# Performance work log

Hardware: AMD Instinct MI355X
Metric: run time of the kernel (lower is better)

## Reference

```python
import jax, jax.numpy as jnp
import numpy as np

HEADS = 16
EPS = 1e-5  # nn.LayerNorm default


def setup_inputs() -> dict:
    key = jax.random.key(0)
    ks = jax.random.split(key, 3)
    b, n, dim = 4, 1024, 1024
    x = jax.random.normal(ks[0], (b, n, dim), jnp.float32)
    ln_gamma = jnp.ones((dim,), jnp.float32)
    ln_beta = jnp.zeros((dim,), jnp.float32)
    # torch.nn.Linear stores weight as [out_features, in_features]
    w_qkv = jax.random.normal(ks[1], (3 * dim, dim), jnp.float32) * (dim ** -0.5)
    w_out = jax.random.normal(ks[2], (dim, dim), jnp.float32) * (dim ** -0.5)
    b_out = jnp.zeros((dim,), jnp.float32)
    return {"x": x, "ln_gamma": ln_gamma, "ln_beta": ln_beta,
            "w_qkv": w_qkv, "w_out": w_out, "b_out": b_out, "topk": 32}


def reference(x, ln_gamma, ln_beta, w_qkv, w_out, b_out, topk):
    b, n, dim = x.shape
    h = HEADS
    d = dim // h
    scale = d ** -0.5  # (inner_dim/heads)^-0.5 with inner_dim=dim

    # LayerNorm (biased variance, matching torch)
    mu = x.mean(-1, keepdims=True)
    var = x.var(-1, keepdims=True)
    xn = (x - mu) * jax.lax.rsqrt(var + EPS) * ln_gamma + ln_beta

    # qkv projection (no bias): y = x @ W^T
    qkv = jnp.einsum('bnd,ed->bne', xn, w_qkv)  # [b, n, 3*dim]
    q, k, v = jnp.split(qkv, 3, axis=-1)
    split_heads = lambda t: t.reshape(b, n, h, d).transpose(0, 2, 1, 3)  # [b,h,n,d]
    q = split_heads(q) * scale
    k = split_heads(k)
    v = split_heads(v)

    sim = jnp.einsum('bhid,bhjd->bhij', q, k)          # [b,h,n,n]
    attn = jax.nn.softmax(sim, axis=-1)
    # top-k SELECTION: probability values are discarded, only indices used
    _, idx = jax.lax.top_k(attn, topk)                 # [b,h,n,topk]
    # gather v rows at top-k indices and sum (unweighted), matching
    # torch.gather(vv, 2, idx).sum(-2)
    gathered = jnp.take_along_axis(
        v, idx.reshape(b, h, n * topk)[..., None], axis=2)  # [b,h,n*topk,d]
    xsum = gathered.reshape(b, h, n, topk, d).sum(axis=3)   # [b,h,n,d]

    # global min/max normalization then exp
    xmin = xsum.min()
    xmax = xsum.max()
    out = jnp.exp((xsum - xmin) / (xmax - xmin))

    out = out.transpose(0, 2, 1, 3).reshape(b, n, dim)  # b h n d -> b n (h d)
    # final projection (self.out Linear; Dropout(0.2) inert at eval)
    return jnp.einsum('bnd,ed->bne', out, w_out) + b_out
```

## Files before the change

kernel.cpp:

```cpp
#include <hip/hip_runtime.h>


#define LN_EPS 1e-5f

using half8   = __attribute__((ext_vector_type(8))) _Float16;
using half4   = __attribute__((ext_vector_type(4))) _Float16;
using float4v = __attribute__((ext_vector_type(4))) float;

__device__ __forceinline__ void gload_lds16(const void* g, void* l) {
  __builtin_amdgcn_global_load_lds(
      (const __attribute__((address_space(1))) void*)g,
      (__attribute__((address_space(3))) void*)l, 16, 0, 0);
}
__device__ __forceinline__ float4v mfma16(half8 a, half8 b, float4v c) {
  return __builtin_amdgcn_mfma_f32_16x16x32_f16(a, b, c, 0, 0, 0);
}
struct HL { _Float16 h, l; };
__device__ __forceinline__ HL split2(float x) {
  _Float16 h = (_Float16)x;
  return { h, (_Float16)(x - (float)h) };
}
__device__ __forceinline__ int mbcnt(unsigned long long m) {
  return __builtin_amdgcn_mbcnt_hi((unsigned)(m >> 32),
         __builtin_amdgcn_mbcnt_lo((unsigned)m, 0u));
}

__device__ __forceinline__ unsigned fkey(float f) {
  unsigned u = __float_as_uint(f);
  return ((int)u < 0) ? ~u : (u | 0x80000000u);
}
__device__ __forceinline__ int enc_i(float f) {
  int i = __float_as_int(f);
  return i >= 0 ? i : (i ^ 0x7fffffff);
}
__device__ __forceinline__ float dec_i(int e) {
  return __int_as_float(e >= 0 ? e : (e ^ 0x7fffffff));
}

__global__ __launch_bounds__(256)
void prep_kernel(const float* __restrict__ x, const float* __restrict__ gamma,
                 const float* __restrict__ beta,
                 _Float16* __restrict__ xh, _Float16* __restrict__ xl,
                 const float* __restrict__ wqkv, const float* __restrict__ wout,
                 _Float16* __restrict__ wqh, _Float16* __restrict__ wql,
                 _Float16* __restrict__ woh,
                 int* __restrict__ pmin, int* __restrict__ pmax) {
  int blk = blockIdx.x, t = threadIdx.x;
  if (blk < 4096) {
    __shared__ float red[8];
    int row = blk;
    const float4* xr = (const float4*)(x + (size_t)row * 1024);
    float4 v = xr[t];
    float s  = v.x + v.y + v.z + v.w;
    float s2 = v.x*v.x + v.y*v.y + v.z*v.z + v.w*v.w;
    #pragma unroll
    for (int o = 32; o >= 1; o >>= 1) {
      s  += __shfl_xor(s,  o, 64);
      s2 += __shfl_xor(s2, o, 64);
    }
    int w = t >> 6, l = t & 63;
    if (l == 0) { red[w*2] = s; red[w*2+1] = s2; }
    __syncthreads();
    float S  = red[0] + red[2] + red[4] + red[6];
    float S2 = red[1] + red[3] + red[5] + red[7];
    float mu  = S * (1.0f/1024.0f);
    float var = S2 * (1.0f/1024.0f) - mu*mu;
    float r = rsqrtf(var + LN_EPS);
    float4 g  = ((const float4*)gamma)[t];
    float4 bb = ((const float4*)beta)[t];
    float o0 = (v.x - mu) * r * g.x + bb.x;
    float o1 = (v.y - mu) * r * g.y + bb.y;
    float o2 = (v.z - mu) * r * g.z + bb.z;
    float o3 = (v.w - mu) * r * g.w + bb.w;
    HL r0 = split2(o0), r1 = split2(o1), r2 = split2(o2), r3 = split2(o3);
    half4 hh = { r0.h, r1.h, r2.h, r3.h };
    half4 ll = { r0.l, r1.l, r2.l, r3.l };
    size_t e = (size_t)row * 1024 + t*4;
    *(half4*)(xh + e) = hh;
    *(half4*)(xl + e) = ll;
  } else if (blk < 8192) {
    size_t i4 = (size_t)(blk - 4096) * 256 + t;
    if (i4 < 786432) {
      float4 v = ((const float4*)wqkv)[i4];
      half4 hh = { (_Float16)v.x, (_Float16)v.y, (_Float16)v.z, (_Float16)v.w };
      ((half4*)wqh)[i4] = hh;
      if (i4 < 524288) {
        HL r0 = split2(v.x), r1 = split2(v.y), r2 = split2(v.z), r3 = split2(v.w);
        half4 ll = { r0.l, r1.l, r2.l, r3.l };
        ((half4*)wql)[i4] = ll;
      }
    } else {
      size_t off = i4 - 786432;
      float4 v = ((const float4*)wout)[off];
      half4 hh = { (_Float16)v.x, (_Float16)v.y, (_Float16)v.z, (_Float16)v.w };
      ((half4*)woh)[off] = hh;
    }
  } else {
    if (t < 64)              pmin[t]      = 0x7fffffff;
    else if (t < 128)        pmax[t - 64] = (int)0x80000000;
  }
}

__global__ __launch_bounds__(256)
void gemm_qkv(const _Float16* __restrict__ Ah, const _Float16* __restrict__ Al,
              const _Float16* __restrict__ Bh, const _Float16* __restrict__ Bl,
              _Float16* __restrict__ QH, _Float16* __restrict__ QL,
              _Float16* __restrict__ KH, _Float16* __restrict__ KL,
              float* __restrict__ CV) {
  __shared__ __align__(16) _Float16 lds[4 * 128 * 32];
  const int K = 1024;
  int tid = threadIdx.x, w = tid >> 6, l = tid & 63;
  int m0 = blockIdx.y * 128, n0 = blockIdx.x * 128;
  int wm = (w >> 1) * 64, wn = (w & 1) * 64;
  bool vblk = (n0 >= 2048);

  const _Float16* src = (w == 0) ? Ah : (w == 1) ? Al : (w == 2) ? Bh : Bl;
  int rowbase = (w < 2) ? m0 : n0;
  _Float16* dst = lds + (size_t)w * 4096;
  int sr = l >> 2, sc = l & 3;
  bool stager = !vblk || (w & 1) == 0;

  float4v acc[4][4];
  #pragma unroll
  for (int u = 0; u < 4; ++u)
    #pragma unroll
    for (int vv = 0; vv < 4; ++vv) acc[u][vv] = (float4v){0.f, 0.f, 0.f, 0.f};

  int quad = l >> 4, lo16 = l & 15;
  for (int kt = 0; kt < K; kt += 32) {
    __syncthreads();
    if (stager) {
      #pragma unroll
      for (int i = 0; i < 8; ++i) {
        int row = i * 16 + sr;
        gload_lds16(src + (size_t)(rowbase + row) * K + kt + sc * 8,
                    dst + row * 32 + sc * 8);
      }
    }
    __syncthreads();
    half8 ah[4], bh[4];
    #pragma unroll
    for (int u = 0; u < 4; ++u) {
      int mrow = wm + u * 16 + lo16;
      int nrow = wn + u * 16 + lo16;
      ah[u] = *(const half8*)&lds[        (size_t)mrow * 32 + quad * 8];
      bh[u] = *(const half8*)&lds[ 8192 + (size_t)nrow * 32 + quad * 8];
    }
    #pragma unroll
    for (int u = 0; u < 4; ++u)
      #pragma unroll
      for (int vv = 0; vv < 4; ++vv)
        acc[u][vv] = mfma16(ah[u], bh[vv], acc[u][vv]);
    if (!vblk) {
      half8 al[4], bl[4];
      #pragma unroll
      for (int u = 0; u < 4; ++u) {
        int mrow = wm + u * 16 + lo16;
        int nrow = wn + u * 16 + lo16;
        al[u] = *(const half8*)&lds[ 4096 + (size_t)mrow * 32 + quad * 8];
        bl[u] = *(const half8*)&lds[12288 + (size_t)nrow * 32 + quad * 8];
      }
      #pragma unroll
      for (int u = 0; u < 4; ++u)
        #pragma unroll
        for (int vv = 0; vv < 4; ++vv)
          acc[u][vv] = mfma16(ah[u], bl[vv], acc[u][vv]);
      #pragma unroll
      for (int u = 0; u < 4; ++u)
        #pragma unroll
        for (int vv = 0; vv < 4; ++vv)
          acc[u][vv] = mfma16(al[u], bh[vv], acc[u][vv]);
    }
  }

  #pragma unroll
  for (int u = 0; u < 4; ++u) {
    #pragma unroll
    for (int vv = 0; vv < 4; ++vv) {
      #pragma unroll
      for (int rg = 0; rg < 4; ++rg) {
        int row = m0 + wm + u * 16 + quad * 4 + rg;
        int col = n0 + wn + vv * 16 + lo16;
        float val = acc[u][vv][rg];
        int which = col >> 10, h = (col >> 6) & 15, dd = col & 63;
        int b = row >> 10, i = row & 1023;
        size_t e = ((size_t)(b * 16 + h) << 16) + ((size_t)i << 6) + dd;
        if (which == 2) { CV[e] = val; }
        else {
          HL sp = split2(val);
          if (which == 0) { QH[e] = sp.h; QL[e] = sp.l; }
          else            { KH[e] = sp.h; KL[e] = sp.l; }
        }
      }
    }
  }
}

__global__ __launch_bounds__(1024, 8)
void attn_kernel(const _Float16* __restrict__ qh, const _Float16* __restrict__ ql,
                 const _Float16* __restrict__ kh, const _Float16* __restrict__ kl,
                 const float* __restrict__ vg, float* __restrict__ xsum,
                 int* __restrict__ pmin, int* __restrict__ pmax) {
  __shared__ unsigned kb[16][1028];
  __shared__ int sel[16][32];
  __shared__ float bmn[16], bmx[16];
  int g = blockIdx.x;
  int xcd = g & 7, slot = g >> 3;
  int bh = (slot >> 6) * 8 + xcd, grp = slot & 63;
  int tid = threadIdx.x, w = tid >> 6, l = tid & 63;
  int quad = l >> 4, lo16 = l & 15;
  size_t hb = (size_t)bh << 16;

  const _Float16* qhp = qh + hb + ((size_t)(grp * 16 + lo16) << 6);
  const _Float16* qlp = ql + hb + ((size_t)(grp * 16 + lo16) << 6);
  half8 ah0 = *(const half8*)(qhp + quad * 8);
  half8 ah1 = *(const half8*)(qhp + 32 + quad * 8);
  half8 al0 = *(const half8*)(qlp + quad * 8);
  half8 al1 = *(const half8*)(qlp + 32 + quad * 8);

  const _Float16* khp = kh + hb;
  const _Float16* klp = kl + hb;
  int jbase = w * 64;

  half8 b0, b1, c0f, c1f, d0, d1, e0, e1;
  {
    size_t off = ((size_t)(jbase + lo16) << 6) + quad * 8;
    b0  = *(const half8*)(khp + off);
    b1  = *(const half8*)(khp + off + 32);
    c0f = *(const half8*)(klp + off);
    c1f = *(const half8*)(klp + off + 32);
  }
  #pragma unroll
  for (int tt = 0; tt < 4; ++tt) {
    if (tt < 3) {
      size_t off = ((size_t)(jbase + (tt + 1) * 16 + lo16) << 6) + quad * 8;
      d0 = *(const half8*)(khp + off);
      d1 = *(const half8*)(khp + off + 32);
      e0 = *(const half8*)(klp + off);
      e1 = *(const half8*)(klp + off + 32);
    }
    float4v acc = (float4v){0.f, 0.f, 0.f, 0.f};
    __builtin_amdgcn_s_setprio(1);
    acc = mfma16(ah0, b0, acc);
    acc = mfma16(ah0, c0f, acc);
    acc = mfma16(al0, b0, acc);
    acc = mfma16(ah1, b1, acc);
    acc = mfma16(ah1, c1f, acc);
    acc = mfma16(al1, b1, acc);
    __builtin_amdgcn_s_setprio(0);
    int jc = jbase + tt * 16 + lo16;
    #pragma unroll
    for (int rg = 0; rg < 4; ++rg)
      kb[quad * 4 + rg][jc] = fkey(acc[rg]);
    b0 = d0; b1 = d1; c0f = e0; c1f = e1;
  }
  __syncthreads();

  unsigned ku[16];
  #pragma unroll
  for (int s = 0; s < 16; ++s) ku[s] = kb[w][s * 64 + l];

  unsigned lmax = ku[0];
  #pragma unroll
  for (int s = 1; s < 16; ++s) lmax = (ku[s] > lmax) ? ku[s] : lmax;
  unsigned rmx = lmax, rmn = lmax;
  #pragma unroll
  for (int o = 32; o >= 1; o >>= 1) {
    unsigned tx = (unsigned)__shfl_xor((int)rmx, o, 64);
    unsigned tn = (unsigned)__shfl_xor((int)rmn, o, 64);
    rmx = (tx > rmx) ? tx : rmx;
    rmn = (tn < rmn) ? tn : rmn;
  }

  unsigned cur;
  bool exact = false;
  unsigned diff = rmx ^ rmn;
  if (diff == 0u) {
    cur = rmx;
  } else {
    int hbit = 31 - __builtin_clz(diff);
    unsigned mask = (hbit == 31) ? 0xffffffffu : ((2u << hbit) - 1u);
    cur = rmx & ~mask;
    for (int bit = hbit; bit >= 0; --bit) {
      unsigned T = cur | (1u << bit);
      int c = 0;
      #pragma unroll
      for (int s = 0; s < 16; ++s) c += __popcll(__ballot(ku[s] >= T));
      if (c >= 32) {
        cur = T;
        if (c == 32) { exact = true; break; }
      }
    }
  }

  int base = 0;
  if (exact) {
    #pragma unroll
    for (int s = 0; s < 16; ++s) {
      bool take = ku[s] >= cur;
      unsigned long long mtk = __ballot(take);
      if (take) sel[w][base + mbcnt(mtk)] = s * 64 + l;
      base += __popcll(mtk);
    }
  } else {
    int gcnt = 0;
    #pragma unroll
    for (int s = 0; s < 16; ++s) gcnt += __popcll(__ballot(ku[s] > cur));
    int need = 32 - gcnt;
    int eqb = 0;
    #pragma unroll
    for (int s = 0; s < 16; ++s) {
      bool gt = ku[s] > cur;
      bool eq = ku[s] == cur;
      unsigned long long meq = __ballot(eq);
      int eqr = eqb + mbcnt(meq);
      bool take = gt || (eq && (eqr < need));
      unsigned long long mtk = __ballot(take);
      if (take) sel[w][base + mbcnt(mtk)] = s * 64 + l;
      base += __popcll(mtk);
      eqb  += __popcll(meq);
    }
  }

  const float* vb = vg + hb;
  int lg = l >> 4, lc = (l & 15) * 4;
  float4 vacc = {0.f, 0.f, 0.f, 0.f};
  #pragma unroll
  for (int p = 0; p < 8; ++p) {
    int j = sel[w][p * 4 + lg];
    float4 t = *(const float4*)(vb + ((size_t)j << 6) + lc);
    vacc.x += t.x; vacc.y += t.y; vacc.z += t.z; vacc.w += t.w;
  }
  #pragma unroll
  for (int o = 32; o >= 16; o >>= 1) {
    vacc.x += __shfl_xor(vacc.x, o, 64);
    vacc.y += __shfl_xor(vacc.y, o, 64);
    vacc.z += __shfl_xor(vacc.z, o, 64);
    vacc.w += __shfl_xor(vacc.w, o, 64);
  }
  if (l < 16)
    *(float4*)(xsum + hb + ((size_t)(grp * 16 + w) << 6) + l * 4) = vacc;

  float m4 = fminf(fminf(vacc.x, vacc.y), fminf(vacc.z, vacc.w));
  float M4 = fmaxf(fmaxf(vacc.x, vacc.y), fmaxf(vacc.z, vacc.w));
  #pragma unroll
  for (int o = 8; o >= 1; o >>= 1) {
    m4 = fminf(m4, __shfl_xor(m4, o, 64));
    M4 = fmaxf(M4, __shfl_xor(M4, o, 64));
  }
  if (l == 0) { bmn[w] = m4; bmx[w] = M4; }
  __syncthreads();
  if (w == 0 && l < 16) {
    float a = bmn[l], b2 = bmx[l];
    #pragma unroll
    for (int o = 8; o >= 1; o >>= 1) {
      a  = fminf(a,  __shfl_xor(a,  o, 64));
      b2 = fmaxf(b2, __shfl_xor(b2, o, 64));
    }
    if (l == 0) {
      atomicMin(pmin + bh, enc_i(a));
      atomicMax(pmax + bh, enc_i(b2));
    }
  }
}

__global__ __launch_bounds__(256)
void fin_kernel(const float* __restrict__ xsum, const int* __restrict__ pmin,
                const int* __restrict__ pmax, _Float16* __restrict__ oh) {
  __shared__ float mm[2];
  int tid = threadIdx.x;
  if (tid < 64) {
    float fa = dec_i(pmin[tid]);
    float fb = dec_i(pmax[tid]);
    #pragma unroll
    for (int o = 32; o >= 1; o >>= 1) {
      fa = fminf(fa, __shfl_xor(fa, o, 64));
      fb = fmaxf(fb, __shfl_xor(fb, o, 64));
    }
    if (tid == 0) { mm[0] = fa; mm[1] = fb; }
  }
  __syncthreads();
  float mn = mm[0];
  float inv = 1.0f / (mm[1] - mn);
  int idx = blockIdx.x * 256 + tid;
  float4 xv = ((const float4*)xsum)[idx];
  half4 hh = { (_Float16)expf((xv.x - mn) * inv),
               (_Float16)expf((xv.y - mn) * inv),
               (_Float16)expf((xv.z - mn) * inv),
               (_Float16)expf((xv.w - mn) * inv) };
  int e0 = idx << 2;
  int bh = e0 >> 16, i = (e0 >> 6) & 1023, dd = e0 & 63;
  int b = bh >> 4, h = bh & 15;
  size_t oe = ((size_t)(b * 1024 + i) << 10) + (h << 6) + dd;
  *(half4*)(oh + oe) = hh;
}

__global__ __launch_bounds__(256)
void gemm_out(const _Float16* __restrict__ A, const _Float16* __restrict__ Bw,
              const float* __restrict__ bias, float* __restrict__ CO) {
  __shared__ __align__(16) _Float16 lds[192 * 32];
  const int K = 1024;
  int tid = threadIdx.x, w = tid >> 6, l = tid & 63;
  int m0 = blockIdx.y * 128, n0 = blockIdx.x * 64;
  int wm = (w >> 1) * 64, wn = (w & 1) * 32;
  int sr = l >> 2, sc = l & 3;
  int quad = l >> 4, lo16 = l & 15;

  float4v acc[4][2];
  #pragma unroll
  for (int u = 0; u < 4; ++u)
    #pragma unroll
    for (int vv = 0; vv < 2; ++vv) acc[u][vv] = (float4v){0.f, 0.f, 0.f, 0.f};

  for (int kt = 0; kt < K; kt += 32) {
    __syncthreads();
    #pragma unroll
    for (int i = 0; i < 3; ++i) {
      int row = w * 48 + i * 16 + sr;
      const _Float16* sp = (row < 128)
          ? A  + (size_t)(m0 + row) * K + kt + sc * 8
          : Bw + (size_t)(n0 + row - 128) * K + kt + sc * 8;
      gload_lds16(sp, lds + row * 32 + sc * 8);
    }
    __syncthreads();
    half8 af[4], bf[2];
    #pragma unroll
    for (int u = 0; u < 4; ++u)
      af[u] = *(const half8*)&lds[(size_t)(wm + u * 16 + lo16) * 32 + quad * 8];
    #pragma unroll
    for (int vv = 0; vv < 2; ++vv)
      bf[vv] = *(const half8*)&lds[(size_t)(128 + wn + vv * 16 + lo16) * 32
                                   + quad * 8];
    #pragma unroll
    for (int u = 0; u < 4; ++u)
      #pragma unroll
      for (int vv = 0; vv < 2; ++vv)
        acc[u][vv] = mfma16(af[u], bf[vv], acc[u][vv]);
  }

  #pragma unroll
  for (int u = 0; u < 4; ++u) {
    #pragma unroll
    for (int vv = 0; vv < 2; ++vv) {
      #pragma unroll
      for (int rg = 0; rg < 4; ++rg) {
        int row = m0 + wm + u * 16 + quad * 4 + rg;
        int col = n0 + wn + vv * 16 + lo16;
        CO[(size_t)row * 1024 + col] = acc[u][vv][rg] + bias[col];
      }
    }
  }
}

extern "C" void kernel_launch(void* const* d_in, const int* in_sizes, int n_in,
                              void* d_out, int out_size, void* d_ws, size_t ws_size,
                              hipStream_t stream) {
  const float* x     = (const float*)d_in[0];
  const float* gamma = (const float*)d_in[1];
  const float* beta  = (const float*)d_in[2];
  const float* w_qkv = (const float*)d_in[3];
  const float* w_out = (const float*)d_in[4];
  const float* b_out = (const float*)d_in[5];

  char* B = (char*)d_ws;
  const size_t MB = 1024ull * 1024ull;
  float*    v   = (float*)B;
  _Float16* qh  = (_Float16*)(B + 16*MB);
  _Float16* ql  = (_Float16*)(B + 24*MB);
  _Float16* kh  = (_Float16*)(B + 32*MB);
  _Float16* kl  = (_Float16*)(B + 40*MB);
  float*    xs  = (float*)(B + 48*MB);
  _Float16* xh  = (_Float16*)(B + 48*MB);
  _Float16* xl  = (_Float16*)(B + 56*MB);
  _Float16* woh = (_Float16*)(B + 64*MB);
  int*     pmin = (int*)(B + 66*MB);
  int*     pmax = (int*)(B + 66*MB + 4096);
  _Float16* wqh = (_Float16*)(B + 69*MB);
  _Float16* wql = (_Float16*)(B + 75*MB);
  _Float16* oth = qh;

  prep_kernel<<<8193, 256, 0, stream>>>(x, gamma, beta, xh, xl,
                                        w_qkv, w_out, wqh, wql, woh,
                                        pmin, pmax);
  gemm_qkv<<<dim3(24, 32), 256, 0, stream>>>(
      xh, xl, wqh, wql, qh, ql, kh, kl, v);
  attn_kernel<<<4096, 1024, 0, stream>>>(qh, ql, kh, kl, v, xs, pmin, pmax);
  fin_kernel<<<4096, 256, 0, stream>>>(xs, pmin, pmax, oth);
  gemm_out<<<dim3(16, 32), 256, 0, stream>>>(oth, woh, b_out, (float*)d_out);
}
```

Baseline: 355.9 us.

## Use fp16-only scores for top-k candidates, then rescore candidates in split precision

The attention score pass now uses only the high fp16 halves of Q and K, which cuts the MFMA work and K loads to a third. The GEMM epilogue computes per-row Q norms and per-head max K norms, which give an error bound. Candidates within that bound of the approximate 32nd score are gathered and rescored exactly with hi/lo fp32 dot products, then ranked. If more than 128 candidates qualify, it falls back to the full three-term MFMA score recompute and the original radix selection. The gains depend on candidate counts staying small, and the GEMM gains an extra epilogue with atomics.

```diff
diff --git a/kernel.cpp b/kernel.cpp
--- a/kernel.cpp
+++ b/kernel.cpp
@@ -28,6 +28,10 @@
 __device__ __forceinline__ unsigned fkey(float f) {
   unsigned u = __float_as_uint(f);
   return ((int)u < 0) ? ~u : (u | 0x80000000u);
+}
+__device__ __forceinline__ float key2f(unsigned k) {
+  return (k & 0x80000000u) ? __uint_as_float(k & 0x7fffffffu)
+                           : __uint_as_float(~k);
 }
 __device__ __forceinline__ int enc_i(float f) {
   int i = __float_as_int(f);
@@ -44,7 +48,8 @@
                  const float* __restrict__ wqkv, const float* __restrict__ wout,
                  _Float16* __restrict__ wqh, _Float16* __restrict__ wql,
                  _Float16* __restrict__ woh,
-                 int* __restrict__ pmin, int* __restrict__ pmax) {
+                 int* __restrict__ pmin, int* __restrict__ pmax,
+                 int* __restrict__ knm) {
   int blk = blockIdx.x, t = threadIdx.x;
   if (blk < 4096) {
     __shared__ float red[8];
@@ -96,8 +101,9 @@
       ((half4*)woh)[off] = hh;
     }
   } else {
-    if (t < 64)              pmin[t]      = 0x7fffffff;
-    else if (t < 128)        pmax[t - 64] = (int)0x80000000;
+    if (t < 64)              pmin[t]       = 0x7fffffff;
+    else if (t < 128)        pmax[t - 64]  = (int)0x80000000;
+    else if (t < 192)        knm[t - 128]  = 0;
   }
 }
 
@@ -106,7 +112,8 @@
               const _Float16* __restrict__ Bh, const _Float16* __restrict__ Bl,
               _Float16* __restrict__ QH, _Float16* __restrict__ QL,
               _Float16* __restrict__ KH, _Float16* __restrict__ KL,
-              float* __restrict__ CV) {
+              float* __restrict__ CV, float* __restrict__ QN,
+              int* __restrict__ KNM) {
   __shared__ __align__(16) _Float16 lds[4 * 128 * 32];
   const int K = 1024;
   int tid = threadIdx.x, w = tid >> 6, l = tid & 63;
@@ -194,13 +201,48 @@
       }
     }
   }
+
+  if (!vblk) {
+    int hh2 = ((n0 + wn) >> 6) & 15;
+    bool isq = (n0 < 1024);
+    float wmax = 0.f;
+    #pragma unroll
+    for (int u = 0; u < 4; ++u) {
+      #pragma unroll
+      for (int rg = 0; rg < 4; ++rg) {
+        float s = 0.f;
+        #pragma unroll
+        for (int vv = 0; vv < 4; ++vv) {
+          float t2 = acc[u][vv][rg];
+          s += t2 * t2;
+        }
+        #pragma unroll
+        for (int o = 8; o >= 1; o >>= 1) s += __shfl_xor(s, o, 64);
+        if (isq) {
+          if (lo16 == 0) {
+            int row = m0 + wm + u * 16 + quad * 4 + rg;
+            QN[((size_t)((row >> 10) * 16 + hh2) << 10) + (row & 1023)] = s;
+          }
+        } else {
+          wmax = fmaxf(wmax, s);
+        }
+      }
+    }
+    if (!isq) {
+      #pragma unroll
+      for (int o = 32; o >= 1; o >>= 1)
+        wmax = fmaxf(wmax, __shfl_xor(wmax, o, 64));
+      if (l == 0) atomicMax(KNM + (m0 >> 10) * 16 + hh2, __float_as_int(wmax));
+    }
+  }
 }
 
 __global__ __launch_bounds__(1024, 8)
 void attn_kernel(const _Float16* __restrict__ qh, const _Float16* __restrict__ ql,
                  const _Float16* __restrict__ kh, const _Float16* __restrict__ kl,
                  const float* __restrict__ vg, float* __restrict__ xsum,
-                 int* __restrict__ pmin, int* __restrict__ pmax) {
+                 int* __restrict__ pmin, int* __restrict__ pmax,
+                 const float* __restrict__ qn, const int* __restrict__ knm) {
   __shared__ unsigned kb[16][1028];
   __shared__ int sel[16][32];
   __shared__ float bmn[16], bmx[16];
@@ -215,20 +257,16 @@
   const _Float16* qlp = ql + hb + ((size_t)(grp * 16 + lo16) << 6);
   half8 ah0 = *(const half8*)(qhp + quad * 8);
   half8 ah1 = *(const half8*)(qhp + 32 + quad * 8);
-  half8 al0 = *(const half8*)(qlp + quad * 8);
-  half8 al1 = *(const half8*)(qlp + 32 + quad * 8);
 
   const _Float16* khp = kh + hb;
   const _Float16* klp = kl + hb;
   int jbase = w * 64;
 
-  half8 b0, b1, c0f, c1f, d0, d1, e0, e1;
+  half8 b0, b1, d0, d1;
   {
     size_t off = ((size_t)(jbase + lo16) << 6) + quad * 8;
-    b0  = *(const half8*)(khp + off);
-    b1  = *(const half8*)(khp + off + 32);
-    c0f = *(const half8*)(klp + off);
-    c1f = *(const half8*)(klp + off + 32);
+    b0 = *(const half8*)(khp + off);
+    b1 = *(const half8*)(khp + off + 32);
   }
   #pragma unroll
   for (int tt = 0; tt < 4; ++tt) {
@@ -236,24 +274,22 @@
       size_t off = ((size_t)(jbase + (tt + 1) * 16 + lo16) << 6) + quad * 8;
       d0 = *(const half8*)(khp + off);
       d1 = *(const half8*)(khp + off + 32);
-      e0 = *(const half8*)(klp + off);
-      e1 = *(const half8*)(klp + off + 32);
     }
     float4v acc = (float4v){0.f, 0.f, 0.f, 0.f};
     __builtin_amdgcn_s_setprio(1);
     acc = mfma16(ah0, b0, acc);
-    acc = mfma16(ah0, c0f, acc);
-    acc = mfma16(al0, b0, acc);
     acc = mfma16(ah1, b1, acc);
-    acc = mfma16(ah1, c1f, acc);
-    acc = mfma16(al1, b1, acc);
     __builtin_amdgcn_s_setprio(0);
     int jc = jbase + tt * 16 + lo16;
     #pragma unroll
     for (int rg = 0; rg < 4; ++rg)
       kb[quad * 4 + rg][jc] = fkey(acc[rg]);
-    b0 = d0; b1 = d1; c0f = e0; c1f = e1;
-  }
+    b0 = d0; b1 = d1;
+  }
+  int rw = grp * 16 + w;
+  float qn2 = qn[((size_t)bh << 10) + rw];
+  float kn2 = __int_as_float(knm[bh]);
+  float eps = 0.002f * sqrtf(qn2 * kn2);
   __syncthreads();
 
   unsigned ku[16];
@@ -271,9 +307,7 @@
     rmx = (tx > rmx) ? tx : rmx;
     rmn = (tn < rmn) ? tn : rmn;
   }
-
   unsigned cur;
-  bool exact = false;
   unsigned diff = rmx ^ rmn;
   if (diff == 0u) {
     cur = rmx;
@@ -288,37 +322,156 @@
       for (int s = 0; s < 16; ++s) c += __popcll(__ballot(ku[s] >= T));
       if (c >= 32) {
         cur = T;
-        if (c == 32) { exact = true; break; }
-      }
-    }
-  }
-
+        if (c == 32) break;
+      }
+    }
+  }
+
+  unsigned tk = fkey(key2f(cur) - 2.0f * eps);
   int base = 0;
-  if (exact) {
-    #pragma unroll
-    for (int s = 0; s < 16; ++s) {
-      bool take = ku[s] >= cur;
-      unsigned long long mtk = __ballot(take);
-      if (take) sel[w][base + mbcnt(mtk)] = s * 64 + l;
-      base += __popcll(mtk);
-    }
+  #pragma unroll
+  for (int s = 0; s < 16; ++s) {
+    bool take = ku[s] >= tk;
+    unsigned long long mtk = __ballot(take);
+    if (take) kb[w][base + mbcnt(mtk)] = (unsigned)(s * 64 + l);
+    base += __popcll(mtk);
+  }
+  int N = base;
+
+  if (N <= 128) {
+    int j0 = (l < N) ? (int)kb[w][l] : -1;
+    int j1 = (64 + l < N) ? (int)kb[w][64 + l] : -1;
+    const _Float16* qrh = qh + hb + ((size_t)rw << 6);
+    const _Float16* qrl = ql + hb + ((size_t)rw << 6);
+    float s0 = 0.f, s1 = 0.f;
+    #pragma unroll
+    for (int db = 0; db < 4; ++db) {
+      half8 qa = *(const half8*)(qrh + db * 16);
+      half8 qb = *(const half8*)(qrh + db * 16 + 8);
+      half8 qc = *(const half8*)(qrl + db * 16);
+      half8 qd = *(const half8*)(qrl + db * 16 + 8);
+      if (j0 >= 0) {
+        const _Float16* kr = khp + ((size_t)j0 << 6) + db * 16;
+        const _Float16* lr = klp + ((size_t)j0 << 6) + db * 16;
+        half8 ka = *(const half8*)kr, kb2 = *(const half8*)(kr + 8);
+        half8 la = *(const half8*)lr, lb2 = *(const half8*)(lr + 8);
+        #pragma unroll
+        for (int e = 0; e < 8; ++e) {
+          float qhf = (float)qa[e], qlf = (float)qc[e];
+          float khf = (float)ka[e], klf = (float)la[e];
+          s0 += qhf * khf + qlf * khf + qhf * klf;
+          qhf = (float)qb[e]; qlf = (float)qd[e];
+          khf = (float)kb2[e]; klf = (float)lb2[e];
+          s0 += qhf * khf + qlf * khf + qhf * klf;
+        }
+      }
+      if (j1 >= 0) {
+        const _Float16* kr = khp + ((size_t)j1 << 6) + db * 16;
+        const _Float16* lr = klp + ((size_t)j1 << 6) + db * 16;
+        half8 ka = *(const half8*)kr, kb2 = *(const half8*)(kr + 8);
+        half8 la = *(const half8*)lr, lb2 = *(const half8*)(lr + 8);
+        #pragma unroll
+        for (int e = 0; e < 8; ++e) {
+          float qhf = (float)qa[e], qlf = (float)qc[e];
+          float khf = (float)ka[e], klf = (float)la[e];
+          s1 += qhf * khf + qlf * khf + qhf * klf;
+          qhf = (float)qb[e]; qlf = (float)qd[e];
+          khf = (float)kb2[e]; klf = (float)lb2[e];
+          s1 += qhf * khf + qlf * khf + qhf * klf;
+        }
+      }
+    }
+    unsigned k0 = fkey(s0), k1 = fkey(s1);
+    kb[w][256 + l] = k0;
+    kb[w][320 + l] = k1;
+    int r0 = 0, r1 = 0;
+    for (int o = 0; o < N; ++o) {
+      unsigned ko = kb[w][256 + o];
+      r0 += (ko > k0) || (ko == k0 && o < l);
+      r1 += (ko > k1) || (ko == k1 && o < 64 + l);
+    }
+    if (j0 >= 0 && r0 < 32) sel[w][r0] = j0;
+    if (j1 >= 0 && r1 < 32) sel[w][r1] = j1;
   } else {
-    int gcnt = 0;
-    #pragma unroll
-    for (int s = 0; s < 16; ++s) gcnt += __popcll(__ballot(ku[s] > cur));
-    int need = 32 - gcnt;
-    int eqb = 0;
-    #pragma unroll
-    for (int s = 0; s < 16; ++s) {
-      bool gt = ku[s] > cur;
-      bool eq = ku[s] == cur;
-      unsigned long long meq = __ballot(eq);
-      int eqr = eqb + mbcnt(meq);
-      bool take = gt || (eq && (eqr < need));
-      unsigned long long mtk = __ballot(take);
-      if (take) sel[w][base + mbcnt(mtk)] = s * 64 + l;
-      base += __popcll(mtk);
-      eqb  += __popcll(meq);
+    half8 al0 = *(const half8*)(qlp + quad * 8);
+    half8 al1 = *(const half8*)(qlp + 32 + quad * 8);
+    int myq = w >> 2, myr = w & 3;
+    for (int jt = 0; jt < 64; ++jt) {
+      size_t off = ((size_t)(jt * 16 + lo16) << 6) + quad * 8;
+      half8 f0 = *(const half8*)(khp + off);
+      half8 f1 = *(const half8*)(khp + off + 32);
+      half8 g0 = *(const half8*)(klp + off);
+      half8 g1 = *(const half8*)(klp + off + 32);
+      float4v a2 = (float4v){0.f, 0.f, 0.f, 0.f};
+      a2 = mfma16(ah0, f0, a2);
+      a2 = mfma16(ah0, g0, a2);
+      a2 = mfma16(al0, f0, a2);
+      a2 = mfma16(ah1, f1, a2);
+      a2 = mfma16(ah1, g1, a2);
+      a2 = mfma16(al1, f1, a2);
+      float xv = myr == 0 ? a2[0] : myr == 1 ? a2[1] : myr == 2 ? a2[2] : a2[3];
+      if (quad == myq) kb[w][jt * 16 + lo16] = fkey(xv);
+    }
+    #pragma unroll
+    for (int s = 0; s < 16; ++s) ku[s] = kb[w][s * 64 + l];
+    unsigned lm2 = ku[0];
+    #pragma unroll
+    for (int s = 1; s < 16; ++s) lm2 = (ku[s] > lm2) ? ku[s] : lm2;
+    unsigned rx = lm2, rn = lm2;
+    #pragma unroll
+    for (int o = 32; o >= 1; o >>= 1) {
+      unsigned tx = (unsigned)__shfl_xor((int)rx, o, 64);
+      unsigned tn = (unsigned)__shfl_xor((int)rn, o, 64);
+      rx = (tx > rx) ? tx : rx;
+      rn = (tn < rn) ? tn : rn;
+    }
+    unsigned cur2;
+    bool exact = false;
+    unsigned df2 = rx ^ rn;
+    if (df2 == 0u) {
+      cur2 = rx;
+    } else {
+      int hbit = 31 - __builtin_clz(df2);
+      unsigned mask = (hbit == 31) ? 0xffffffffu : ((2u << hbit) - 1u);
+      cur2 = rx & ~mask;
+      for (int bit = hbit; bit >= 0; --bit) {
+        unsigned T = cur2 | (1u << bit);
+        int c = 0;
+        #pragma unroll
+        for (int s = 0; s < 16; ++s) c += __popcll(__ballot(ku[s] >= T));
+        if (c >= 32) {
+          cur2 = T;
+          if (c == 32) { exact = true; break; }
+        }
+      }
+    }
+    int b2 = 0;
+    if (exact) {
+      #pragma unroll
+      for (int s = 0; s < 16; ++s) {
+        bool take = ku[s] >= cur2;
+        unsigned long long mtk = __ballot(take);
+        if (take) sel[w][b2 + mbcnt(mtk)] = s * 64 + l;
+        b2 += __popcll(mtk);
+      }
+    } else {
+      int gcnt = 0;
+      #pragma unroll
+      for (int s = 0; s < 16; ++s) gcnt += __popcll(__ballot(ku[s] > cur2));
+      int need = 32 - gcnt;
+      int eqb = 0;
+      #pragma unroll
+      for (int s = 0; s < 16; ++s) {
+        bool gt = ku[s] > cur2;
+        bool eq = ku[s] == cur2;
+        unsigned long long meq = __ballot(eq);
+        int eqr = eqb + mbcnt(meq);
+        bool take = gt || (eq && (eqr < need));
+        unsigned long long mtk = __ballot(take);
+        if (take) sel[w][b2 + mbcnt(mtk)] = s * 64 + l;
+        b2 += __popcll(mtk);
+        eqb += __popcll(meq);
+      }
     }
   }
 
@@ -339,7 +492,7 @@
     vacc.w += __shfl_xor(vacc.w, o, 64);
   }
   if (l < 16)
-    *(float4*)(xsum + hb + ((size_t)(grp * 16 + w) << 6) + l * 4) = vacc;
+    *(float4*)(xsum + hb + ((size_t)rw << 6) + l * 4) = vacc;
 
   float m4 = fminf(fminf(vacc.x, vacc.y), fminf(vacc.z, vacc.w));
   float M4 = fmaxf(fmaxf(vacc.x, vacc.y), fmaxf(vacc.z, vacc.w));
@@ -351,15 +504,15 @@
   if (l == 0) { bmn[w] = m4; bmx[w] = M4; }
   __syncthreads();
   if (w == 0 && l < 16) {
-    float a = bmn[l], b2 = bmx[l];
+    float a = bmn[l], b3 = bmx[l];
     #pragma unroll
     for (int o = 8; o >= 1; o >>= 1) {
       a  = fminf(a,  __shfl_xor(a,  o, 64));
-      b2 = fmaxf(b2, __shfl_xor(b2, o, 64));
+      b3 = fmaxf(b3, __shfl_xor(b3, o, 64));
     }
     if (l == 0) {
       atomicMin(pmin + bh, enc_i(a));
-      atomicMax(pmax + bh, enc_i(b2));
+      atomicMax(pmax + bh, enc_i(b3));
     }
   }
 }
@@ -475,16 +628,19 @@
   _Float16* woh = (_Float16*)(B + 64*MB);
   int*     pmin = (int*)(B + 66*MB);
   int*     pmax = (int*)(B + 66*MB + 4096);
+  int*     knm  = (int*)(B + 66*MB + 8192);
+  float*   qn   = (float*)(B + 67*MB);
   _Float16* wqh = (_Float16*)(B + 69*MB);
   _Float16* wql = (_Float16*)(B + 75*MB);
   _Float16* oth = qh;
 
   prep_kernel<<<8193, 256, 0, stream>>>(x, gamma, beta, xh, xl,
                                         w_qkv, w_out, wqh, wql, woh,
-                                        pmin, pmax);
+                                        pmin, pmax, knm);
   gemm_qkv<<<dim3(24, 32), 256, 0, stream>>>(
-      xh, xl, wqh, wql, qh, ql, kh, kl, v);
-  attn_kernel<<<4096, 1024, 0, stream>>>(qh, ql, kh, kl, v, xs, pmin, pmax);
+      xh, xl, wqh, wql, qh, ql, kh, kl, v, qn, knm);
+  attn_kernel<<<4096, 1024, 0, stream>>>(qh, ql, kh, kl, v, xs,
+                                         pmin, pmax, qn, knm);
   fin_kernel<<<4096, 256, 0, stream>>>(xs, pmin, pmax, oth);
   gemm_out<<<dim3(16, 32), 256, 0, stream>>>(oth, woh, b_out, (float*)d_out);
 }
```

Measured after the change: 585.8 us. +64.6%, slower.
